# Kernel tuning notes

Hardware: AMD Instinct MI355X
Metric: run time of the kernel (lower is better)

The kernel has to match this reference:

```python
import jax, jax.numpy as jnp
import numpy as np

DIM = 512
HEADS = 8
DIM_HEAD = 64
HIDDEN = HEADS * DIM_HEAD  # 512
B, N, M = 4, 2048, 2048


def setup_inputs() -> dict:
    key = jax.random.key(0)
    ks = jax.random.split(key, 7)
    s = 0.02
    return {
        "x": jax.random.normal(ks[0], (B, N, DIM), jnp.float32),
        "context": jax.random.normal(ks[1], (B, M, DIM), jnp.float32),
        "Wq": jax.random.normal(ks[2], (DIM, HIDDEN), jnp.float32) * s,
        "Wk": jax.random.normal(ks[3], (DIM, HIDDEN), jnp.float32) * s,
        "Wv": jax.random.normal(ks[4], (DIM, HIDDEN), jnp.float32) * s,
        "Wo": jax.random.normal(ks[5], (HIDDEN, DIM), jnp.float32) * s,
        "bo": jnp.zeros((DIM,), jnp.float32),
    }


def reference(x, context, Wq, Wk, Wv, Wo, bo):
    scale = DIM_HEAD ** (-0.5)
    # projections: [B, N, HIDDEN] -> [B, H, N, D]
    def split_heads(t):
        b, n, _ = t.shape
        return t.reshape(b, n, HEADS, DIM_HEAD).transpose(0, 2, 1, 3)
    q = split_heads(x @ Wq)
    k = split_heads(context @ Wk)
    v = split_heads(context @ Wv)
    # scores: [B, H, N, M]
    sim = jnp.einsum('bhid,bhjd->bhij', q, k) * scale
    attn = jax.nn.softmax(sim, axis=-1)
    out = jnp.einsum('bhij,bhjd->bhid', attn, v)  # [B, H, N, D]
    out = out.transpose(0, 2, 1, 3).reshape(x.shape[0], x.shape[1], HIDDEN)
    return out @ Wo + bo
```

## Files before the change

kernel.cpp:

```cpp
#include <hip/hip_runtime.h>
#include <hip/hip_bf16.h>


typedef __attribute__((ext_vector_type(8))) short bf16x8;
typedef __attribute__((ext_vector_type(4))) float f32x4;

#define MFMA16(a, b, c) __builtin_amdgcn_mfma_f32_16x16x32_bf16(a, b, c, 0, 0, 0)
#define SCALE_LOG2E 0.18033688011112042f

static __device__ inline unsigned short f2b(float f) {
    __hip_bfloat16 h = __float2bfloat16(f);
    return __builtin_bit_cast(unsigned short, h);
}
static __device__ inline unsigned int pk_rnd(float hi, float lo) {
    unsigned uh = __builtin_bit_cast(unsigned, hi) + 0x8000u;
    unsigned ul = __builtin_bit_cast(unsigned, lo) + 0x8000u;
    return __builtin_amdgcn_perm(uh, ul, 0x07060302);
}
static __device__ inline float fexp2(float x) {
    float r;
    asm("v_exp_f32 %0, %1" : "=v"(r) : "v"(x));
    return r;
}
static __device__ inline void gll16(const void* g, void* l) {
    __builtin_amdgcn_global_load_lds(
        (const __attribute__((address_space(1))) void*)g,
        (__attribute__((address_space(3))) void*)l, 16, 0, 0);
}

__global__ __launch_bounds__(256) void prep_kernel(const float* __restrict__ x,
                                                   const float* __restrict__ ctx,
                                                   const float* __restrict__ Wq,
                                                   const float* __restrict__ Wk,
                                                   const float* __restrict__ Wv,
                                                   const float* __restrict__ Wo,
                                                   unsigned short* __restrict__ xb,
                                                   unsigned short* __restrict__ cb,
                                                   unsigned short* __restrict__ wt_base) {
    __shared__ float T[64][65];
    const int bid = blockIdx.x, tid = threadIdx.x;
    if (bid < 8192) {
        const float* src = (bid < 4096) ? x : ctx;
        unsigned short* dst = (bid < 4096) ? xb : cb;
        int i = (bid & 4095) * 256 + tid;
        const float4 v = reinterpret_cast<const float4*>(src)[i];
        uint2 o;
        o.x = pk_rnd(v.y, v.x);
        o.y = pk_rnd(v.w, v.z);
        reinterpret_cast<uint2*>(dst)[i] = o;
        return;
    }
    const int b = bid - 8192;
    const int which = b >> 6, t6 = b & 63;
    const float* W = (which == 0) ? Wq : (which == 1) ? Wk : (which == 2) ? Wv : Wo;
    unsigned short* Wt = wt_base + (size_t)which * 512 * 512;
    const int n0 = (t6 & 7) * 64, k0 = (t6 >> 3) * 64;
    const int rr = tid >> 4, cc = (tid & 15) * 4;
    #pragma unroll
    for (int i = 0; i < 4; i++) {
        const float4 v = *reinterpret_cast<const float4*>(&W[(size_t)(k0 + rr + 16 * i) * 512 + n0 + cc]);
        T[rr + 16 * i][cc + 0] = v.x; T[rr + 16 * i][cc + 1] = v.y;
        T[rr + 16 * i][cc + 2] = v.z; T[rr + 16 * i][cc + 3] = v.w;
    }
    __syncthreads();
    #pragma unroll
    for (int i = 0; i < 4; i++) {
        int n = rr + 16 * i;
        uint2 o;
        o.x = pk_rnd(T[cc + 1][n], T[cc + 0][n]);
        o.y = pk_rnd(T[cc + 3][n], T[cc + 2][n]);
        *reinterpret_cast<uint2*>(&Wt[(size_t)(n0 + n) * 512 + k0 + cc]) = o;
    }
}

__device__ inline void gemm_tile_128(const unsigned short* __restrict__ A,
                                     const unsigned short* __restrict__ Bt,
                                     int row0, int col0, f32x4 acc[4][4]) {
    __shared__ unsigned short As[128 * 32];
    __shared__ unsigned short Bs[128 * 32];
    const int tid  = threadIdx.x;
    const int lane = tid & 63, wave = tid >> 6;
    const int quad = lane >> 4, mr = lane & 15;
    const int m_off = (wave & 1) * 64, n_off = (wave >> 1) * 64;

    const int lrow = lane >> 2;
    const int lq   = (lane & 3) ^ (lrow & 3);
    const unsigned short* aSrc = A  + (size_t)(row0 + wave * 32 + lrow) * 512 + lq * 8;
    const unsigned short* bSrc = Bt + (size_t)(col0 + wave * 32 + lrow) * 512 + lq * 8;
    unsigned short* aL0 = &As[(wave * 32) * 32];
    unsigned short* aL1 = &As[(wave * 32 + 16) * 32];
    unsigned short* bL0 = &Bs[(wave * 32) * 32];
    unsigned short* bL1 = &Bs[(wave * 32 + 16) * 32];

    for (int kt = 0; kt < 16; kt++) {
        __syncthreads();
        gll16(aSrc + kt * 32, aL0);
        gll16(aSrc + 16 * 512 + kt * 32, aL1);
        gll16(bSrc + kt * 32, bL0);
        gll16(bSrc + 16 * 512 + kt * 32, bL1);
        __syncthreads();
        bf16x8 af[4], bfr[4];
        #pragma unroll
        for (int i = 0; i < 4; i++) {
            int m = m_off + i * 16 + mr;
            af[i] = *reinterpret_cast<const bf16x8*>(&As[m * 32 + ((quad ^ (m & 3)) * 8)]);
        }
        #pragma unroll
        for (int j = 0; j < 4; j++) {
            int n = n_off + j * 16 + mr;
            bfr[j] = *reinterpret_cast<const bf16x8*>(&Bs[n * 32 + ((quad ^ (n & 3)) * 8)]);
        }
        #pragma unroll
        for (int i = 0; i < 4; i++)
            #pragma unroll
            for (int j = 0; j < 4; j++)
                acc[i][j] = MFMA16(af[i], bfr[j], acc[i][j]);
    }
}

__global__ __launch_bounds__(256) void gemm_proj_kernel(const unsigned short* __restrict__ xb,
                                                        const unsigned short* __restrict__ cb,
                                                        const unsigned short* __restrict__ wt_base,
                                                        unsigned short* __restrict__ qkv_base) {
    const int f = blockIdx.x, g = f & 7, j = f >> 3;
    const int xt = j & 3;
    const int ry = g + 8 * ((j >> 2) & 7);
    const int which = j >> 5;

    const unsigned short* A  = (which == 0) ? xb : cb;
    const unsigned short* Bt = wt_base + (size_t)which * 512 * 512;
    unsigned short* out      = qkv_base + (size_t)which * 8192 * 512;

    f32x4 acc[4][4];
    #pragma unroll
    for (int i = 0; i < 4; i++)
        #pragma unroll
        for (int j2 = 0; j2 < 4; j2++) acc[i][j2] = (f32x4){0.f, 0.f, 0.f, 0.f};

    gemm_tile_128(A, Bt, ry * 128, xt * 128, acc);

    const int lane = threadIdx.x & 63, wave = threadIdx.x >> 6;
    const int quad = lane >> 4, mr = lane & 15;
    const int m_off = (wave & 1) * 64, n_off = (wave >> 1) * 64;
    const float qs = (which == 0) ? SCALE_LOG2E : 1.0f;

    if (which == 2) {
        #pragma unroll
        for (int i = 0; i < 4; i++) {
            #pragma unroll
            for (int j2 = 0; j2 < 4; j2++) {
                int gcol = xt * 128 + n_off + j2 * 16 + mr;
                int h = gcol >> 6, d = gcol & 63;
                int grow = ry * 128 + m_off + i * 16 + quad * 4;
                int b = grow >> 11, n = grow & 2047;
                int np = (n & ~31) | (((n >> 2) & 3) << 3) | (((n >> 4) & 1) << 2);
                uint2 o;
                o.x = pk_rnd(acc[i][j2][1], acc[i][j2][0]);
                o.y = pk_rnd(acc[i][j2][3], acc[i][j2][2]);
                *reinterpret_cast<uint2*>(&out[((size_t)(b * 8 + h) * 64 + d) * 2048 + np]) = o;
            }
        }
    } else {
        #pragma unroll
        for (int i = 0; i < 4; i++) {
            #pragma unroll
            for (int j2 = 0; j2 < 4; j2++) {
                int gcol = xt * 128 + n_off + j2 * 16 + mr;
                int h = gcol >> 6, d = gcol & 63;
                #pragma unroll
                for (int r = 0; r < 4; r++) {
                    int grow = ry * 128 + m_off + i * 16 + quad * 4 + r;
                    int b = grow >> 11, n = grow & 2047;
                    out[((size_t)(b * 8 + h) * 2048 + n) * 64 + d] = f2b(acc[i][j2][r] * qs);
                }
            }
        }
    }
}

__global__ __launch_bounds__(256) void flash_kernel(const unsigned short* __restrict__ qw,
                                                    const unsigned short* __restrict__ kw,
                                                    const unsigned short* __restrict__ vt,
                                                    float* __restrict__ p0,
                                                    float* __restrict__ p1,
                                                    float* __restrict__ l0,
                                                    float* __restrict__ l1) {
    __shared__ unsigned short Ks[64 * 72];
    __shared__ unsigned short Vs[64 * 72];

    const int f = blockIdx.x, g = f & 7, j = f >> 3;
    const int qtile = j & 15;
    const int kidx  = (j >> 4) & 1;
    const int bh    = g + 8 * (j >> 5);

    const int tid  = threadIdx.x;
    const int lane = tid & 63, wave = tid >> 6;
    const int quad = lane >> 4, mr = lane & 15;

    const unsigned short* qbase = qw + ((size_t)bh * 2048 + qtile * 128 + wave * 32) * 64;
    const unsigned short* kbase = kw + (size_t)bh * 2048 * 64;
    const unsigned short* vbase = vt + (size_t)bh * 64 * 2048;
    float* Pdst = kidx ? p1 : p0;
    float* ldst = kidx ? l1 : l0;

    bf16x8 qf[2][2];
    #pragma unroll
    for (int gq = 0; gq < 2; gq++) {
        qf[gq][0] = *reinterpret_cast<const bf16x8*>(qbase + (gq * 16 + mr) * 64 + quad * 8);
        qf[gq][1] = *reinterpret_cast<const bf16x8*>(qbase + (gq * 16 + mr) * 64 + 32 + quad * 8);
    }

    bf16x8 ones;
    #pragma unroll
    for (int e = 0; e < 8; e++) ones[e] = (short)0x3F80;

    f32x4 oacc[2][4], lacc[2];
    #pragma unroll
    for (int gq = 0; gq < 2; gq++) {
        lacc[gq] = (f32x4){0.f, 0.f, 0.f, 0.f};
        #pragma unroll
        for (int nt = 0; nt < 4; nt++) oacc[gq][nt] = (f32x4){0.f, 0.f, 0.f, 0.f};
    }

    const int srow = tid >> 2, soff = (tid & 3) * 16;

    const int kbeg = kidx * 1024;
    for (int key0 = kbeg; key0 < kbeg + 1024; key0 += 64) {
        __syncthreads();
        {
            const uint4* kp = reinterpret_cast<const uint4*>(kbase + (size_t)(key0 + srow) * 64 + soff);
            uint4* kd = reinterpret_cast<uint4*>(&Ks[srow * 72 + soff]);
            kd[0] = kp[0]; kd[1] = kp[1];
            const uint4* vp = reinterpret_cast<const uint4*>(vbase + (size_t)srow * 2048 + key0 + soff);
            uint4* vd = reinterpret_cast<uint4*>(&Vs[srow * 72 + soff]);
            vd[0] = vp[0]; vd[1] = vp[1];
        }
        __syncthreads();

        f32x4 sv[2][4];
        #pragma unroll
        for (int gq = 0; gq < 2; gq++)
            #pragma unroll
            for (int kt = 0; kt < 4; kt++) sv[gq][kt] = (f32x4){0.f, 0.f, 0.f, 0.f};
        #pragma unroll
        for (int c = 0; c < 2; c++) {
            #pragma unroll
            for (int kt = 0; kt < 4; kt++) {
                bf16x8 kf = *reinterpret_cast<const bf16x8*>(&Ks[(kt * 16 + mr) * 72 + c * 32 + quad * 8]);
                sv[0][kt] = MFMA16(kf, qf[0][c], sv[0][kt]);
                sv[1][kt] = MFMA16(kf, qf[1][c], sv[1][kt]);
            }
        }

        bf16x8 pa[2][2];
        #pragma unroll
        for (int gq = 0; gq < 2; gq++) {
            #pragma unroll
            for (int ks = 0; ks < 2; ks++) {
                uint4 w;
                w.x = pk_rnd(fexp2(sv[gq][2 * ks][1]),     fexp2(sv[gq][2 * ks][0]));
                w.y = pk_rnd(fexp2(sv[gq][2 * ks][3]),     fexp2(sv[gq][2 * ks][2]));
                w.z = pk_rnd(fexp2(sv[gq][2 * ks + 1][1]), fexp2(sv[gq][2 * ks + 1][0]));
                w.w = pk_rnd(fexp2(sv[gq][2 * ks + 1][3]), fexp2(sv[gq][2 * ks + 1][2]));
                pa[gq][ks] = __builtin_bit_cast(bf16x8, w);
            }
        }

        #pragma unroll
        for (int ks = 0; ks < 2; ks++) {
            lacc[0] = MFMA16(pa[0][ks], ones, lacc[0]);
            lacc[1] = MFMA16(pa[1][ks], ones, lacc[1]);
            #pragma unroll
            for (int nt = 0; nt < 4; nt++) {
                bf16x8 vf = *reinterpret_cast<const bf16x8*>(&Vs[(nt * 16 + mr) * 72 + ks * 32 + quad * 8]);
                oacc[0][nt] = MFMA16(pa[0][ks], vf, oacc[0][nt]);
                oacc[1][nt] = MFMA16(pa[1][ks], vf, oacc[1][nt]);
            }
        }
    }

    const int b = bh >> 3, h = bh & 7;
    #pragma unroll
    for (int gq = 0; gq < 2; gq++) {
        #pragma unroll
        for (int nt = 0; nt < 4; nt++) {
            #pragma unroll
            for (int r = 0; r < 4; r++) {
                int row = qtile * 128 + wave * 32 + gq * 16 + quad * 4 + r;
                Pdst[((size_t)b * 2048 + row) * 512 + h * 64 + nt * 16 + mr] = oacc[gq][nt][r];
            }
        }
        if (mr == 0) {
            #pragma unroll
            for (int r = 0; r < 4; r++) {
                int row = qtile * 128 + wave * 32 + gq * 16 + quad * 4 + r;
                ldst[(size_t)bh * 2048 + row] = lacc[gq][r];
            }
        }
    }
}

__global__ __launch_bounds__(256) void combine_kernel(const float* __restrict__ p0,
                                                      const float* __restrict__ p1,
                                                      const float* __restrict__ l0,
                                                      const float* __restrict__ l1,
                                                      unsigned short* __restrict__ ob) {
    const int idx = blockIdx.x * 256 + threadIdx.x;
    const size_t flat = (size_t)idx * 4;
    const int row = (int)(flat >> 9);
    const int c   = (int)(flat & 511);
    const int bh  = (row >> 11) * 8 + (c >> 6);
    const int qn  = row & 2047;
    const float lv = l0[(size_t)bh * 2048 + qn] + l1[(size_t)bh * 2048 + qn];
    const float li = 1.0f / lv;
    const float4 a = reinterpret_cast<const float4*>(p0)[idx];
    const float4 bb = reinterpret_cast<const float4*>(p1)[idx];
    uint2 o;
    o.x = pk_rnd((a.y + bb.y) * li, (a.x + bb.x) * li);
    o.y = pk_rnd((a.w + bb.w) * li, (a.z + bb.z) * li);
    reinterpret_cast<uint2*>(ob)[idx] = o;
}

__global__ __launch_bounds__(256) void gemm_out_kernel(const unsigned short* __restrict__ obuf,
                                                       const unsigned short* __restrict__ Wot,
                                                       const float* __restrict__ bo,
                                                       float* __restrict__ out) {
    const int f = blockIdx.x, g = f & 7, j = f >> 3;
    const int xt = j & 3;
    const int ry = g + 8 * (j >> 2);

    f32x4 acc[4][4];
    #pragma unroll
    for (int i = 0; i < 4; i++)
        #pragma unroll
        for (int j2 = 0; j2 < 4; j2++) acc[i][j2] = (f32x4){0.f, 0.f, 0.f, 0.f};

    gemm_tile_128(obuf, Wot, ry * 128, xt * 128, acc);

    const int lane = threadIdx.x & 63, wave = threadIdx.x >> 6;
    const int quad = lane >> 4, mr = lane & 15;
    const int m_off = (wave & 1) * 64, n_off = (wave >> 1) * 64;
    #pragma unroll
    for (int i = 0; i < 4; i++) {
        #pragma unroll
        for (int j2 = 0; j2 < 4; j2++) {
            int gcol = xt * 128 + n_off + j2 * 16 + mr;
            float bias = bo[gcol];
            #pragma unroll
            for (int r = 0; r < 4; r++) {
                int grow = ry * 128 + m_off + i * 16 + quad * 4 + r;
                out[(size_t)grow * 512 + gcol] = acc[i][j2][r] + bias;
            }
        }
    }
}

extern "C" void kernel_launch(void* const* d_in, const int* in_sizes, int n_in,
                              void* d_out, int out_size, void* d_ws, size_t ws_size,
                              hipStream_t stream) {
    const float* x   = (const float*)d_in[0];
    const float* ctx = (const float*)d_in[1];
    const float* Wq  = (const float*)d_in[2];
    const float* Wk  = (const float*)d_in[3];
    const float* Wv  = (const float*)d_in[4];
    const float* Wo  = (const float*)d_in[5];
    const float* bo  = (const float*)d_in[6];
    float* out = (float*)d_out;

    unsigned short* ws  = (unsigned short*)d_ws;
    unsigned short* xb  = ws;
    unsigned short* cb  = xb + (size_t)8192 * 512;
    unsigned short* Wt  = cb + (size_t)8192 * 512;
    unsigned short* qkv = Wt + (size_t)4 * 512 * 512;
    unsigned short* ob  = qkv + (size_t)3 * 8192 * 512;

    float* p0 = out;
    float* p1 = (float*)xb;
    float* l0 = (float*)Wt;
    float* l1 = (float*)(Wt + (size_t)512 * 512);

    prep_kernel<<<8448, 256, 0, stream>>>(x, ctx, Wq, Wk, Wv, Wo, xb, cb, Wt);
    gemm_proj_kernel<<<768, 256, 0, stream>>>(xb, cb, Wt, qkv);
    flash_kernel<<<1024, 256, 0, stream>>>(qkv, qkv + (size_t)8192 * 512,
                                           qkv + (size_t)2 * 8192 * 512, p0, p1, l0, l1);
    combine_kernel<<<4096, 256, 0, stream>>>(p0, p1, l0, l1, ob);
    gemm_out_kernel<<<256, 256, 0, stream>>>(ob, Wt + (size_t)3 * 512 * 512, bo, out);
}
```

Baseline: 188.8 us.

## Drop split-K flash attention, fuse normalization, add register-staged K/V double buffer

The flash kernel now processes all 2048 keys per block instead of splitting them into two halves, so the fp32 partial outputs, the row sums and the separate combine kernel are gone, and the normalized bf16 output is written directly. K/V tiles are prefetched into registers one iteration ahead and stored into double-buffered shared memory, which leaves one barrier per iteration. This removes a kernel launch and large fp32 intermediate traffic. In exchange the grid halves to 512 blocks, which lowers parallelism and occupancy on the GPU. The softmax still uses no running max, as before.

```diff
diff --git a/kernel.cpp b/kernel.cpp
--- a/kernel.cpp
+++ b/kernel.cpp
@@ -181,17 +181,13 @@
 __global__ __launch_bounds__(256) void flash_kernel(const unsigned short* __restrict__ qw,
                                                     const unsigned short* __restrict__ kw,
                                                     const unsigned short* __restrict__ vt,
-                                                    float* __restrict__ p0,
-                                                    float* __restrict__ p1,
-                                                    float* __restrict__ l0,
-                                                    float* __restrict__ l1) {
-    __shared__ unsigned short Ks[64 * 72];
-    __shared__ unsigned short Vs[64 * 72];
+                                                    unsigned short* __restrict__ ob) {
+    __shared__ unsigned short Ks[2][64 * 72];
+    __shared__ unsigned short Vs[2][64 * 72];
 
     const int f = blockIdx.x, g = f & 7, j = f >> 3;
     const int qtile = j & 15;
-    const int kidx  = (j >> 4) & 1;
-    const int bh    = g + 8 * (j >> 5);
+    const int bh    = g + 8 * (j >> 4);
 
     const int tid  = threadIdx.x;
     const int lane = tid & 63, wave = tid >> 6;
@@ -200,8 +196,6 @@
     const unsigned short* qbase = qw + ((size_t)bh * 2048 + qtile * 128 + wave * 32) * 64;
     const unsigned short* kbase = kw + (size_t)bh * 2048 * 64;
     const unsigned short* vbase = vt + (size_t)bh * 64 * 2048;
-    float* Pdst = kidx ? p1 : p0;
-    float* ldst = kidx ? l1 : l0;
 
     bf16x8 qf[2][2];
     #pragma unroll
@@ -223,19 +217,33 @@
     }
 
     const int srow = tid >> 2, soff = (tid & 3) * 16;
-
-    const int kbeg = kidx * 1024;
-    for (int key0 = kbeg; key0 < kbeg + 1024; key0 += 64) {
+    const unsigned short* ksrc = kbase + (size_t)srow * 64 + soff;
+    const unsigned short* vsrc = vbase + (size_t)srow * 2048 + soff;
+
+    uint4 ka, kb2, va, vb2;
+    {
+        const uint4* kp = reinterpret_cast<const uint4*>(ksrc);
+        ka = kp[0]; kb2 = kp[1];
+        const uint4* vp = reinterpret_cast<const uint4*>(vsrc);
+        va = vp[0]; vb2 = vp[1];
+    }
+
+    #pragma unroll 2
+    for (int t = 0; t < 32; ++t) {
+        const int cur = t & 1;
+        {
+            uint4* kd = reinterpret_cast<uint4*>(&Ks[cur][srow * 72 + soff]);
+            kd[0] = ka; kd[1] = kb2;
+            uint4* vd = reinterpret_cast<uint4*>(&Vs[cur][srow * 72 + soff]);
+            vd[0] = va; vd[1] = vb2;
+        }
+        if (t < 31) {
+            const uint4* kp = reinterpret_cast<const uint4*>(ksrc + (size_t)(t + 1) * 64 * 64);
+            ka = kp[0]; kb2 = kp[1];
+            const uint4* vp = reinterpret_cast<const uint4*>(vsrc + (t + 1) * 64);
+            va = vp[0]; vb2 = vp[1];
+        }
         __syncthreads();
-        {
-            const uint4* kp = reinterpret_cast<const uint4*>(kbase + (size_t)(key0 + srow) * 64 + soff);
-            uint4* kd = reinterpret_cast<uint4*>(&Ks[srow * 72 + soff]);
-            kd[0] = kp[0]; kd[1] = kp[1];
-            const uint4* vp = reinterpret_cast<const uint4*>(vbase + (size_t)srow * 2048 + key0 + soff);
-            uint4* vd = reinterpret_cast<uint4*>(&Vs[srow * 72 + soff]);
-            vd[0] = vp[0]; vd[1] = vp[1];
-        }
-        __syncthreads();
 
         f32x4 sv[2][4];
         #pragma unroll
@@ -246,7 +254,7 @@
         for (int c = 0; c < 2; c++) {
             #pragma unroll
             for (int kt = 0; kt < 4; kt++) {
-                bf16x8 kf = *reinterpret_cast<const bf16x8*>(&Ks[(kt * 16 + mr) * 72 + c * 32 + quad * 8]);
+                bf16x8 kf = *reinterpret_cast<const bf16x8*>(&Ks[cur][(kt * 16 + mr) * 72 + c * 32 + quad * 8]);
                 sv[0][kt] = MFMA16(kf, qf[0][c], sv[0][kt]);
                 sv[1][kt] = MFMA16(kf, qf[1][c], sv[1][kt]);
             }
@@ -272,7 +280,7 @@
             lacc[1] = MFMA16(pa[1][ks], ones, lacc[1]);
             #pragma unroll
             for (int nt = 0; nt < 4; nt++) {
-                bf16x8 vf = *reinterpret_cast<const bf16x8*>(&Vs[(nt * 16 + mr) * 72 + ks * 32 + quad * 8]);
+                bf16x8 vf = *reinterpret_cast<const bf16x8*>(&Vs[cur][(nt * 16 + mr) * 72 + ks * 32 + quad * 8]);
                 oacc[0][nt] = MFMA16(pa[0][ks], vf, oacc[0][nt]);
                 oacc[1][nt] = MFMA16(pa[1][ks], vf, oacc[1][nt]);
             }
@@ -283,42 +291,15 @@
     #pragma unroll
     for (int gq = 0; gq < 2; gq++) {
         #pragma unroll
-        for (int nt = 0; nt < 4; nt++) {
-            #pragma unroll
-            for (int r = 0; r < 4; r++) {
-                int row = qtile * 128 + wave * 32 + gq * 16 + quad * 4 + r;
-                Pdst[((size_t)b * 2048 + row) * 512 + h * 64 + nt * 16 + mr] = oacc[gq][nt][r];
-            }
-        }
-        if (mr == 0) {
-            #pragma unroll
-            for (int r = 0; r < 4; r++) {
-                int row = qtile * 128 + wave * 32 + gq * 16 + quad * 4 + r;
-                ldst[(size_t)bh * 2048 + row] = lacc[gq][r];
-            }
-        }
-    }
-}
-
-__global__ __launch_bounds__(256) void combine_kernel(const float* __restrict__ p0,
-                                                      const float* __restrict__ p1,
-                                                      const float* __restrict__ l0,
-                                                      const float* __restrict__ l1,
-                                                      unsigned short* __restrict__ ob) {
-    const int idx = blockIdx.x * 256 + threadIdx.x;
-    const size_t flat = (size_t)idx * 4;
-    const int row = (int)(flat >> 9);
-    const int c   = (int)(flat & 511);
-    const int bh  = (row >> 11) * 8 + (c >> 6);
-    const int qn  = row & 2047;
-    const float lv = l0[(size_t)bh * 2048 + qn] + l1[(size_t)bh * 2048 + qn];
-    const float li = 1.0f / lv;
-    const float4 a = reinterpret_cast<const float4*>(p0)[idx];
-    const float4 bb = reinterpret_cast<const float4*>(p1)[idx];
-    uint2 o;
-    o.x = pk_rnd((a.y + bb.y) * li, (a.x + bb.x) * li);
-    o.y = pk_rnd((a.w + bb.w) * li, (a.z + bb.z) * li);
-    reinterpret_cast<uint2*>(ob)[idx] = o;
+        for (int r = 0; r < 4; r++) {
+            const float li = 1.0f / lacc[gq][r];
+            const int row = qtile * 128 + wave * 32 + gq * 16 + quad * 4 + r;
+            unsigned short* orow = &ob[((size_t)b * 2048 + row) * 512 + h * 64 + mr];
+            #pragma unroll
+            for (int nt = 0; nt < 4; nt++)
+                orow[nt * 16] = f2b(oacc[gq][nt][r] * li);
+        }
+    }
 }
 
 __global__ __launch_bounds__(256) void gemm_out_kernel(const unsigned short* __restrict__ obuf,
@@ -374,15 +355,9 @@
     unsigned short* qkv = Wt + (size_t)4 * 512 * 512;
     unsigned short* ob  = qkv + (size_t)3 * 8192 * 512;
 
-    float* p0 = out;
-    float* p1 = (float*)xb;
-    float* l0 = (float*)Wt;
-    float* l1 = (float*)(Wt + (size_t)512 * 512);
-
     prep_kernel<<<8448, 256, 0, stream>>>(x, ctx, Wq, Wk, Wv, Wo, xb, cb, Wt);
     gemm_proj_kernel<<<768, 256, 0, stream>>>(xb, cb, Wt, qkv);
-    flash_kernel<<<1024, 256, 0, stream>>>(qkv, qkv + (size_t)8192 * 512,
-                                           qkv + (size_t)2 * 8192 * 512, p0, p1, l0, l1);
-    combine_kernel<<<4096, 256, 0, stream>>>(p0, p1, l0, l1, ob);
+    flash_kernel<<<512, 256, 0, stream>>>(qkv, qkv + (size_t)8192 * 512,
+                                          qkv + (size_t)2 * 8192 * 512, ob);
     gemm_out_kernel<<<256, 256, 0, stream>>>(ob, Wt + (size_t)3 * 512 * 512, bo, out);
 }
```

Result: faster. 173.5 us (-8.1%).
